# Optimization experiments

Hardware: AMD Instinct MI355X
Metric: run time of the kernel (lower is better)

Reference implementation:

```python
import jax, jax.numpy as jnp
import numpy as np

N_NODES = 100000
N_EDGES = 3200000
IN_DIM = 768
HIDDEN = 128
CLASS_NUM = 2
N_GRAPHS = 512


def setup_inputs() -> dict:
    key = jax.random.key(0)
    ks = jax.random.split(key, 10)
    x = jax.random.normal(ks[0], (N_NODES, IN_DIM), dtype=jnp.float32)
    edge_index = jax.random.randint(ks[1], (2, N_EDGES), 0, N_NODES, dtype=jnp.int64)
    ptr = jnp.sort(jax.random.randint(ks[2], (N_GRAPHS + 1,), 0, N_NODES, dtype=jnp.int64))
    def glorot(k, shape):
        lim = jnp.sqrt(6.0 / (shape[0] + shape[1]))
        return jax.random.uniform(k, shape, jnp.float32, -lim, lim)
    W1 = glorot(ks[3], (IN_DIM, HIDDEN))
    b1 = jnp.zeros((HIDDEN,), jnp.float32)
    W2 = glorot(ks[4], (HIDDEN, HIDDEN))
    b2 = jnp.zeros((HIDDEN,), jnp.float32)
    Wc = glorot(ks[5], (HIDDEN, CLASS_NUM))
    bc = jnp.zeros((CLASS_NUM,), jnp.float32)
    return {"x": x, "edge_index": edge_index, "ptr": ptr,
            "W1": W1, "b1": b1, "W2": W2, "b2": b2, "Wc": Wc, "bc": bc}


def _gcn_conv(x, W, b, src, dst, norm, n_nodes):
    # PyG GCNConv: linear first, then normalized scatter-add aggregation, then bias
    h = x @ W                                  # [N, out]
    msg = h[src] * norm[:, None]               # gather + scale, [E+N, out]
    out = jax.ops.segment_sum(msg, dst, num_segments=n_nodes)
    return out + b


def reference(x, edge_index, ptr, W1, b1, W2, b2, Wc, bc):
    n = x.shape[0]
    loop = jnp.arange(n, dtype=edge_index.dtype)
    src = jnp.concatenate([edge_index[0], loop])  # add self-loops
    dst = jnp.concatenate([edge_index[1], loop])
    deg = jax.ops.segment_sum(jnp.ones_like(dst, dtype=x.dtype), dst, num_segments=n)
    dinv = jnp.where(deg > 0, jax.lax.rsqrt(deg), 0.0)
    norm = dinv[src] * dinv[dst]               # symmetric normalization
    h = jax.nn.relu(_gcn_conv(x, W1, b1, src, dst, norm, n))
    h = jax.nn.relu(_gcn_conv(h, W2, b2, src, dst, norm, n))
    out = _gcn_conv(h, Wc, bc, src, dst, norm, n)
    return out[ptr[:-1]]                       # first_pool: first node of each graph
```

## Files before the change

kernel.cpp:

```cpp
#include <hip/hip_runtime.h>

typedef short bf16x8 __attribute__((ext_vector_type(8)));
typedef float f32x4 __attribute__((ext_vector_type(4)));
typedef _Float16 f16x4 __attribute__((ext_vector_type(4)));

__device__ __forceinline__ unsigned short f2bf_rn(float x) {
    unsigned int u = __float_as_uint(x);
    unsigned int r = u + 0x7FFF + ((u >> 16) & 1);
    return (unsigned short)(r >> 16);
}
__device__ __forceinline__ float bf2f(unsigned short h) {
    return __uint_as_float(((unsigned int)h) << 16);
}


__global__ __launch_bounds__(256) void bucket_hist(const int* __restrict__ ei,
                                                   int* __restrict__ bcnt, int E, int NB) {
    __shared__ int h[1024];
    for (int i = threadIdx.x; i < NB; i += 256) h[i] = 0;
    __syncthreads();
    for (int e = blockIdx.x * blockDim.x + threadIdx.x; e < E; e += gridDim.x * blockDim.x) {
        atomicAdd(&h[ei[E + e] >> 7], 1);
    }
    __syncthreads();
    for (int i = threadIdx.x; i < NB; i += 256) {
        int v = h[i];
        if (v) atomicAdd(&bcnt[i], v);
    }
}

__global__ __launch_bounds__(1024) void bucket_scan(const int* __restrict__ bcnt,
                                                    int* __restrict__ bbase,
                                                    int* __restrict__ bcur,
                                                    int* __restrict__ offs,
                                                    int NB, int NN, int E) {
    __shared__ int s[1024];
    int t = threadIdx.x;
    int v = (t < NB) ? bcnt[t] : 0;
    s[t] = v;
    __syncthreads();
    for (int off = 1; off < 1024; off <<= 1) {
        int u = (t >= off) ? s[t - off] : 0;
        __syncthreads();
        s[t] += u;
        __syncthreads();
    }
    if (t < NB) {
        int base = s[t] - v;
        bbase[t] = base;
        bcur[t] = base;
    }
    if (t == 0) {
        bbase[NB] = E;
        offs[NN] = E;
    }
}

__global__ __launch_bounds__(256) void bucket_scatter(const int* __restrict__ ei,
                                                      int* __restrict__ bcur,
                                                      unsigned int* __restrict__ epk,
                                                      int E, int NB) {
    __shared__ int hist[1024];
    __shared__ int cur[1024];
    int tid = threadIdx.x;
    int chunk = (E + gridDim.x - 1) / gridDim.x;
    int beg = blockIdx.x * chunk;
    int end = beg + chunk; if (end > E) end = E;
    for (int i = tid; i < NB; i += 256) hist[i] = 0;
    __syncthreads();
    for (int e = beg + tid; e < end; e += 256) {
        atomicAdd(&hist[ei[E + e] >> 7], 1);
    }
    __syncthreads();
    for (int i = tid; i < NB; i += 256) {
        int c = hist[i];
        cur[i] = c ? atomicAdd(&bcur[i], c) : 0;
    }
    __syncthreads();
    for (int e = beg + tid; e < end; e += 256) {
        int s = ei[e];
        int d = ei[E + e];
        int p = atomicAdd(&cur[d >> 7], 1);
        epk[p] = ((unsigned)(d & 127) << 17) | (unsigned)s;
    }
}

__global__ __launch_bounds__(256) void bucket_build(const unsigned int* __restrict__ epk,
                                                    const int* __restrict__ bbase,
                                                    int* __restrict__ offs,
                                                    float* __restrict__ dinv,
                                                    int* __restrict__ srt,
                                                    int NN) {
    __shared__ int lcnt[128];
    __shared__ int sc[128];
    __shared__ int lcur[128];
    int b = blockIdx.x;
    int tid = threadIdx.x;
    int base = bbase[b], endp = bbase[b + 1];
    int ne = endp - base;
    int v0 = b << 7;
    int nv = NN - v0; if (nv > 128) nv = 128;

    if (tid < 128) lcnt[tid] = 0;
    __syncthreads();
    for (int i = tid; i < ne; i += 256) {
        int d = (int)(epk[base + i] >> 17);
        atomicAdd(&lcnt[d], 1);
    }
    __syncthreads();
    if (tid < 128) sc[tid] = lcnt[tid];
    __syncthreads();
    for (int off = 1; off < 128; off <<= 1) {
        int u = (tid < 128 && tid >= off) ? sc[tid - off] : 0;
        __syncthreads();
        if (tid < 128) sc[tid] += u;
        __syncthreads();
    }
    if (tid < nv) {
        int ex = sc[tid] - lcnt[tid];
        offs[v0 + tid] = base + ex;
        lcur[tid] = base + ex;
        dinv[v0 + tid] = rsqrtf((float)(lcnt[tid] + 1));
    }
    __syncthreads();
    for (int i = tid; i < ne; i += 256) {
        unsigned int pk = epk[base + i];
        int d = (int)(pk >> 17);
        int s = (int)(pk & 0x1FFFFu);
        int p = atomicAdd(&lcur[d], 1);
        srt[p] = s;
    }
}

__global__ void wt_prep(const float* __restrict__ W, unsigned short* __restrict__ hi,
                        unsigned short* __restrict__ lo, int K) {
    int idx = blockIdx.x * 256 + threadIdx.x;
    if (idx >= K * 128) return;
    int k = idx >> 7;
    int c = idx & 127;
    float x = W[idx];
    unsigned short h = f2bf_rn(x);
    unsigned short l = f2bf_rn(x - bf2f(h));
    hi[(size_t)c * K + k] = h;
    lo[(size_t)c * K + k] = l;
}

template <int K>
__global__ __launch_bounds__(256) void gemm_mfma(const float* __restrict__ X,
                                                 const unsigned short* __restrict__ Wt_hi,
                                                 const unsigned short* __restrict__ Wt_lo,
                                                 const float* __restrict__ dinv,
                                                 _Float16* __restrict__ G, int n) {
    __shared__ unsigned short As_hi[128][40];
    __shared__ unsigned short As_lo[128][40];
    __shared__ unsigned short Bs_hi[128][40];
    __shared__ unsigned short Bs_lo[128][40];

    const int tid = threadIdx.x;
    const int wave = tid >> 6;
    const int lane = tid & 63;
    const int l15 = lane & 15;
    const int l4 = lane >> 4;
    const int row0 = blockIdx.x * 128;
    const int wr0 = wave * 32;

    f32x4 acc[2][8];
#pragma unroll
    for (int i = 0; i < 2; ++i)
#pragma unroll
        for (int j = 0; j < 8; ++j) acc[i][j] = (f32x4){0.f, 0.f, 0.f, 0.f};

    const int sr = tid >> 1;
    const int sf = (tid & 1) * 16;

    for (int k0 = 0; k0 < K; k0 += 32) {
        __syncthreads();
        {
            int grow = row0 + sr;
            float4 v[4];
            if (grow < n) {
                const float* src = X + (size_t)grow * K + k0 + sf;
#pragma unroll
                for (int g = 0; g < 4; ++g) v[g] = *(const float4*)(src + g * 4);
            } else {
#pragma unroll
                for (int g = 0; g < 4; ++g) v[g] = make_float4(0.f, 0.f, 0.f, 0.f);
            }
#pragma unroll
            for (int g = 0; g < 4; ++g) {
                ushort4 h, l;
                h.x = f2bf_rn(v[g].x); l.x = f2bf_rn(v[g].x - bf2f(h.x));
                h.y = f2bf_rn(v[g].y); l.y = f2bf_rn(v[g].y - bf2f(h.y));
                h.z = f2bf_rn(v[g].z); l.z = f2bf_rn(v[g].z - bf2f(h.z));
                h.w = f2bf_rn(v[g].w); l.w = f2bf_rn(v[g].w - bf2f(h.w));
                *(ushort4*)&As_hi[sr][sf + g * 4] = h;
                *(ushort4*)&As_lo[sr][sf + g * 4] = l;
            }
        }
        {
#pragma unroll
            for (int rep = 0; rep < 2; ++rep) {
                int id = tid + rep * 256;
                int c = id >> 2;
                int q = (id & 3) * 8;
                *(uint4*)&Bs_hi[c][q] = *(const uint4*)&Wt_hi[(size_t)c * K + k0 + q];
                *(uint4*)&Bs_lo[c][q] = *(const uint4*)&Wt_lo[(size_t)c * K + k0 + q];
            }
        }
        __syncthreads();
        bf16x8 ah[2], al[2];
#pragma unroll
        for (int i = 0; i < 2; ++i) {
            ah[i] = *(const bf16x8*)&As_hi[wr0 + i * 16 + l15][l4 * 8];
            al[i] = *(const bf16x8*)&As_lo[wr0 + i * 16 + l15][l4 * 8];
        }
#pragma unroll
        for (int j = 0; j < 8; ++j) {
            bf16x8 bh = *(const bf16x8*)&Bs_hi[j * 16 + l15][l4 * 8];
            bf16x8 bl = *(const bf16x8*)&Bs_lo[j * 16 + l15][l4 * 8];
#pragma unroll
            for (int i = 0; i < 2; ++i) {
                acc[i][j] = __builtin_amdgcn_mfma_f32_16x16x32_bf16(ah[i], bh, acc[i][j], 0, 0, 0);
                acc[i][j] = __builtin_amdgcn_mfma_f32_16x16x32_bf16(ah[i], bl, acc[i][j], 0, 0, 0);
                acc[i][j] = __builtin_amdgcn_mfma_f32_16x16x32_bf16(al[i], bh, acc[i][j], 0, 0, 0);
            }
        }
    }
#pragma unroll
    for (int i = 0; i < 2; ++i) {
#pragma unroll
        for (int r = 0; r < 4; ++r) {
            int grow = row0 + wr0 + i * 16 + l4 * 4 + r;
            if (grow < n) {
                float dv = dinv[grow];
#pragma unroll
                for (int j = 0; j < 8; ++j) {
                    G[(size_t)grow * 128 + j * 16 + l15] = (_Float16)(acc[i][j][r] * dv);
                }
            }
        }
    }
}

__global__ __launch_bounds__(256) void aggregate_kernel(const _Float16* __restrict__ G,
                                                        const int* __restrict__ offs,
                                                        const int* __restrict__ srt,
                                                        const float* __restrict__ dinv,
                                                        const float* __restrict__ bias,
                                                        float* __restrict__ H, int n, int do_relu) {
    int wid = (blockIdx.x * blockDim.x + threadIdx.x) >> 6;
    int lane = threadIdx.x & 63;
    if (wid >= n) return;
    int hh = lane >> 5;
    int c4 = (lane & 31) * 4;
    int beg = offs[wid], end = offs[wid + 1];
    float ax = 0.f, ay = 0.f, az = 0.f, aw = 0.f;
    if (!hh) {
        f16x4 s = *(const f16x4*)&G[(size_t)wid * 128 + c4];
        ax = (float)s[0]; ay = (float)s[1]; az = (float)s[2]; aw = (float)s[3];
    }
    int e = beg + hh;
    for (; e + 6 < end; e += 8) {
        int s0 = srt[e], s1 = srt[e + 2], s2 = srt[e + 4], s3 = srt[e + 6];
        f16x4 v0 = *(const f16x4*)&G[(size_t)s0 * 128 + c4];
        f16x4 v1 = *(const f16x4*)&G[(size_t)s1 * 128 + c4];
        f16x4 v2 = *(const f16x4*)&G[(size_t)s2 * 128 + c4];
        f16x4 v3 = *(const f16x4*)&G[(size_t)s3 * 128 + c4];
        ax += (float)v0[0] + (float)v1[0] + (float)v2[0] + (float)v3[0];
        ay += (float)v0[1] + (float)v1[1] + (float)v2[1] + (float)v3[1];
        az += (float)v0[2] + (float)v1[2] + (float)v2[2] + (float)v3[2];
        aw += (float)v0[3] + (float)v1[3] + (float)v2[3] + (float)v3[3];
    }
    for (; e < end; e += 2) {
        int s = srt[e];
        f16x4 v = *(const f16x4*)&G[(size_t)s * 128 + c4];
        ax += (float)v[0]; ay += (float)v[1]; az += (float)v[2]; aw += (float)v[3];
    }
    ax += __shfl_xor(ax, 32);
    ay += __shfl_xor(ay, 32);
    az += __shfl_xor(az, 32);
    aw += __shfl_xor(aw, 32);
    if (!hh) {
        float dv = dinv[wid];
        float4 b = *(const float4*)&bias[c4];
        float4 r;
        r.x = ax * dv + b.x;
        r.y = ay * dv + b.y;
        r.z = az * dv + b.z;
        r.w = aw * dv + b.w;
        if (do_relu) {
            r.x = fmaxf(r.x, 0.f); r.y = fmaxf(r.y, 0.f);
            r.z = fmaxf(r.z, 0.f); r.w = fmaxf(r.w, 0.f);
        }
        *(float4*)&H[(size_t)wid * 128 + c4] = r;
    }
}

__global__ __launch_bounds__(256) void gemm_c2_kernel(const float* __restrict__ H,
                                                      const float* __restrict__ Wc,
                                                      const float* __restrict__ dinv,
                                                      float* __restrict__ G3, int n) {
    int wid = (blockIdx.x * blockDim.x + threadIdx.x) >> 6;
    int lane = threadIdx.x & 63;
    if (wid >= n) return;
    float2 h = *(const float2*)&H[(size_t)wid * 128 + lane * 2];
    float w00 = Wc[lane * 4 + 0];
    float w01 = Wc[lane * 4 + 1];
    float w10 = Wc[lane * 4 + 2];
    float w11 = Wc[lane * 4 + 3];
    float p0 = h.x * w00 + h.y * w10;
    float p1 = h.x * w01 + h.y * w11;
    for (int off = 32; off > 0; off >>= 1) {
        p0 += __shfl_xor(p0, off);
        p1 += __shfl_xor(p1, off);
    }
    if (lane == 0) {
        float dv = dinv[wid];
        G3[(size_t)wid * 2 + 0] = p0 * dv;
        G3[(size_t)wid * 2 + 1] = p1 * dv;
    }
}

__global__ __launch_bounds__(64) void final_kernel(const float* __restrict__ G3,
                                                   const int* __restrict__ ptr,
                                                   const int* __restrict__ offs,
                                                   const int* __restrict__ srt,
                                                   const float* __restrict__ dinv,
                                                   const float* __restrict__ bc,
                                                   float* __restrict__ out, int ngraphs) {
    int i = blockIdx.x;
    if (i >= ngraphs) return;
    int v = ptr[i];
    int lane = threadIdx.x;
    float p0 = 0.f, p1 = 0.f;
    int beg = offs[v], end = offs[v + 1];
    for (int e = beg + lane; e < end; e += 64) {
        int s = srt[e];
        p0 += G3[(size_t)s * 2 + 0];
        p1 += G3[(size_t)s * 2 + 1];
    }
    for (int off = 32; off > 0; off >>= 1) {
        p0 += __shfl_xor(p0, off);
        p1 += __shfl_xor(p1, off);
    }
    if (lane == 0) {
        p0 += G3[(size_t)v * 2 + 0];
        p1 += G3[(size_t)v * 2 + 1];
        float dv = dinv[v];
        out[i * 2 + 0] = p0 * dv + bc[0];
        out[i * 2 + 1] = p1 * dv + bc[1];
    }
}

extern "C" void kernel_launch(void* const* d_in, const int* in_sizes, int n_in,
                              void* d_out, int out_size, void* d_ws, size_t ws_size,
                              hipStream_t stream) {
    const float* x  = (const float*)d_in[0];
    const int* ei   = (const int*)d_in[1];
    const int* ptr  = (const int*)d_in[2];
    const float* W1 = (const float*)d_in[3];
    const float* b1 = (const float*)d_in[4];
    const float* W2 = (const float*)d_in[5];
    const float* b2 = (const float*)d_in[6];
    const float* Wc = (const float*)d_in[7];
    const float* bc = (const float*)d_in[8];
    float* out = (float*)d_out;

    const int IN_DIM = 768, HID = 128;
    const int NN = in_sizes[0] / IN_DIM;
    const int E  = in_sizes[1] / 2;
    const int NG = in_sizes[2] - 1;
    const int NB = (NN + 127) >> 7;

    char* ws = (char*)d_ws;
    size_t off = 0;
    auto alloc = [&](size_t bytes) -> void* {
        void* p = ws + off;
        off += (bytes + 255) & ~(size_t)255;
        return p;
    };
    float* dinv   = (float*)alloc((size_t)NN * 4);
    int*   offs   = (int*)alloc((size_t)(NN + 1) * 4);
    int*   bcnt   = (int*)alloc((size_t)(NB + 1) * 4);
    int*   bbase  = (int*)alloc((size_t)(NB + 1) * 4);
    int*   bcur   = (int*)alloc((size_t)NB * 4);
    int*   srt    = (int*)alloc((size_t)E * 4);
    _Float16* G   = (_Float16*)alloc((size_t)NN * HID * 2);
    float* H      = (float*)alloc((size_t)NN * HID * 4);
    float* G3     = (float*)alloc((size_t)NN * 2 * 4);
    unsigned short* Wt1_hi = (unsigned short*)alloc((size_t)IN_DIM * HID * 2);
    unsigned short* Wt1_lo = (unsigned short*)alloc((size_t)IN_DIM * HID * 2);
    unsigned short* Wt2_hi = (unsigned short*)alloc((size_t)HID * HID * 2);
    unsigned short* Wt2_lo = (unsigned short*)alloc((size_t)HID * HID * 2);

    unsigned int* epk = (unsigned int*)H;

    (void)n_in; (void)out_size; (void)ws_size;

    hipMemsetAsync(bcnt, 0, (size_t)(NB + 1) * 4, stream);
    bucket_hist<<<512, 256, 0, stream>>>(ei, bcnt, E, NB);
    bucket_scan<<<1, 1024, 0, stream>>>(bcnt, bbase, bcur, offs, NB, NN, E);
    bucket_scatter<<<256, 256, 0, stream>>>(ei, bcur, epk, E, NB);
    bucket_build<<<NB, 256, 0, stream>>>(epk, bbase, offs, dinv, srt, NN);

    wt_prep<<<(IN_DIM * HID + 255) / 256, 256, 0, stream>>>(W1, Wt1_hi, Wt1_lo, IN_DIM);
    wt_prep<<<(HID * HID + 255) / 256, 256, 0, stream>>>(W2, Wt2_hi, Wt2_lo, HID);

    int gblocks = (NN + 127) / 128;
    int agg_blocks = (NN * 64 + 255) / 256;

    gemm_mfma<768><<<gblocks, 256, 0, stream>>>(x, Wt1_hi, Wt1_lo, dinv, G, NN);
    aggregate_kernel<<<agg_blocks, 256, 0, stream>>>(G, offs, srt, dinv, b1, H, NN, 1);
    gemm_mfma<128><<<gblocks, 256, 0, stream>>>(H, Wt2_hi, Wt2_lo, dinv, G, NN);
    aggregate_kernel<<<agg_blocks, 256, 0, stream>>>(G, offs, srt, dinv, b2, H, NN, 1);
    gemm_c2_kernel<<<agg_blocks, 256, 0, stream>>>(H, Wc, dinv, G3, NN);
    final_kernel<<<NG, 64, 0, stream>>>(G3, ptr, offs, srt, dinv, bc, out, NG);
}
```

Measured before the change: 520.1 us.

## Store GEMM output in column-sliced planes and aggregate per slice

The GEMM epilogue now writes G as 8 planes of 16 half-precision columns each, instead of row-major 128-wide rows. Aggregation launches 8 blocks per group of 4 nodes, one per column slice, so that concurrently running blocks gather from a smaller 3.2MB plane. The aim is better L2 locality for the random neighbour gathers. In exchange, each gather becomes a 32-byte segment per edge, the CSR index list is read 8 times, and the GEMM epilogue stores are more scattered.

```diff
diff --git a/kernel.cpp b/kernel.cpp
--- a/kernel.cpp
+++ b/kernel.cpp
@@ -2,7 +2,7 @@
 
 typedef short bf16x8 __attribute__((ext_vector_type(8)));
 typedef float f32x4 __attribute__((ext_vector_type(4)));
-typedef _Float16 f16x4 __attribute__((ext_vector_type(4)));
+typedef _Float16 f16x2 __attribute__((ext_vector_type(2)));
 
 __device__ __forceinline__ unsigned short f2bf_rn(float x) {
     unsigned int u = __float_as_uint(x);
@@ -163,6 +163,7 @@
     const int l4 = lane >> 4;
     const int row0 = blockIdx.x * 128;
     const int wr0 = wave * 32;
+    const size_t plane = (size_t)n * 16;
 
     f32x4 acc[2][8];
 #pragma unroll
@@ -235,64 +236,56 @@
                 float dv = dinv[grow];
 #pragma unroll
                 for (int j = 0; j < 8; ++j) {
-                    G[(size_t)grow * 128 + j * 16 + l15] = (_Float16)(acc[i][j][r] * dv);
+                    G[plane * j + (size_t)grow * 16 + l15] = (_Float16)(acc[i][j][r] * dv);
                 }
             }
         }
     }
 }
 
-__global__ __launch_bounds__(256) void aggregate_kernel(const _Float16* __restrict__ G,
-                                                        const int* __restrict__ offs,
-                                                        const int* __restrict__ srt,
-                                                        const float* __restrict__ dinv,
-                                                        const float* __restrict__ bias,
-                                                        float* __restrict__ H, int n, int do_relu) {
-    int wid = (blockIdx.x * blockDim.x + threadIdx.x) >> 6;
+__global__ __launch_bounds__(256) void aggregate_slice(const _Float16* __restrict__ G,
+                                                       const int* __restrict__ offs,
+                                                       const int* __restrict__ srt,
+                                                       const float* __restrict__ dinv,
+                                                       const float* __restrict__ bias,
+                                                       float* __restrict__ H, int n, int do_relu) {
+    int bid = blockIdx.x;
+    int slice = bid & 7;
+    int node = (bid >> 3) * 4 + (threadIdx.x >> 6);
+    if (node >= n) return;
     int lane = threadIdx.x & 63;
-    if (wid >= n) return;
-    int hh = lane >> 5;
-    int c4 = (lane & 31) * 4;
-    int beg = offs[wid], end = offs[wid + 1];
-    float ax = 0.f, ay = 0.f, az = 0.f, aw = 0.f;
-    if (!hh) {
-        f16x4 s = *(const f16x4*)&G[(size_t)wid * 128 + c4];
-        ax = (float)s[0]; ay = (float)s[1]; az = (float)s[2]; aw = (float)s[3];
-    }
-    int e = beg + hh;
-    for (; e + 6 < end; e += 8) {
-        int s0 = srt[e], s1 = srt[e + 2], s2 = srt[e + 4], s3 = srt[e + 6];
-        f16x4 v0 = *(const f16x4*)&G[(size_t)s0 * 128 + c4];
-        f16x4 v1 = *(const f16x4*)&G[(size_t)s1 * 128 + c4];
-        f16x4 v2 = *(const f16x4*)&G[(size_t)s2 * 128 + c4];
-        f16x4 v3 = *(const f16x4*)&G[(size_t)s3 * 128 + c4];
-        ax += (float)v0[0] + (float)v1[0] + (float)v2[0] + (float)v3[0];
-        ay += (float)v0[1] + (float)v1[1] + (float)v2[1] + (float)v3[1];
-        az += (float)v0[2] + (float)v1[2] + (float)v2[2] + (float)v3[2];
-        aw += (float)v0[3] + (float)v1[3] + (float)v2[3] + (float)v3[3];
-    }
-    for (; e < end; e += 2) {
+    int pairId = lane & 7;
+    int slot = lane >> 3;
+    const f16x2* Gp = (const f16x2*)(G + (size_t)slice * (size_t)n * 16);
+    int beg = offs[node], end = offs[node + 1];
+    float a0 = 0.f, a1 = 0.f;
+    int e = beg + slot;
+    for (; e + 8 < end; e += 16) {
+        int s0 = srt[e], s1 = srt[e + 8];
+        f16x2 v0 = Gp[(size_t)s0 * 8 + pairId];
+        f16x2 v1 = Gp[(size_t)s1 * 8 + pairId];
+        a0 += (float)v0[0] + (float)v1[0];
+        a1 += (float)v0[1] + (float)v1[1];
+    }
+    if (e < end) {
         int s = srt[e];
-        f16x4 v = *(const f16x4*)&G[(size_t)s * 128 + c4];
-        ax += (float)v[0]; ay += (float)v[1]; az += (float)v[2]; aw += (float)v[3];
-    }
-    ax += __shfl_xor(ax, 32);
-    ay += __shfl_xor(ay, 32);
-    az += __shfl_xor(az, 32);
-    aw += __shfl_xor(aw, 32);
-    if (!hh) {
-        float dv = dinv[wid];
-        float4 b = *(const float4*)&bias[c4];
-        float4 r;
-        r.x = ax * dv + b.x;
-        r.y = ay * dv + b.y;
-        r.z = az * dv + b.z;
-        r.w = aw * dv + b.w;
-        if (do_relu) {
-            r.x = fmaxf(r.x, 0.f); r.y = fmaxf(r.y, 0.f);
-            r.z = fmaxf(r.z, 0.f); r.w = fmaxf(r.w, 0.f);
-        }
-        *(float4*)&H[(size_t)wid * 128 + c4] = r;
+        f16x2 v = Gp[(size_t)s * 8 + pairId];
+        a0 += (float)v[0];
+        a1 += (float)v[1];
+    }
+    a0 += __shfl_xor(a0, 8);  a1 += __shfl_xor(a1, 8);
+    a0 += __shfl_xor(a0, 16); a1 += __shfl_xor(a1, 16);
+    a0 += __shfl_xor(a0, 32); a1 += __shfl_xor(a1, 32);
+    if (lane < 8) {
+        f16x2 sv = Gp[(size_t)node * 8 + lane];
+        a0 += (float)sv[0];
+        a1 += (float)sv[1];
+        float dv = dinv[node];
+        float2 b = *(const float2*)&bias[slice * 16 + lane * 2];
+        float r0 = a0 * dv + b.x;
+        float r1 = a1 * dv + b.y;
+        if (do_relu) { r0 = fmaxf(r0, 0.f); r1 = fmaxf(r1, 0.f); }
+        *(float2*)&H[(size_t)node * 128 + slice * 16 + lane * 2] = make_float2(r0, r1);
     }
 }
 
@@ -407,12 +400,13 @@
     wt_prep<<<(HID * HID + 255) / 256, 256, 0, stream>>>(W2, Wt2_hi, Wt2_lo, HID);
 
     int gblocks = (NN + 127) / 128;
-    int agg_blocks = (NN * 64 + 255) / 256;
+    int slice_blocks = ((NN + 3) / 4) * 8;
+    int wpn_blocks = (NN * 64 + 255) / 256;
 
     gemm_mfma<768><<<gblocks, 256, 0, stream>>>(x, Wt1_hi, Wt1_lo, dinv, G, NN);
-    aggregate_kernel<<<agg_blocks, 256, 0, stream>>>(G, offs, srt, dinv, b1, H, NN, 1);
+    aggregate_slice<<<slice_blocks, 256, 0, stream>>>(G, offs, srt, dinv, b1, H, NN, 1);
     gemm_mfma<128><<<gblocks, 256, 0, stream>>>(H, Wt2_hi, Wt2_lo, dinv, G, NN);
-    aggregate_kernel<<<agg_blocks, 256, 0, stream>>>(G, offs, srt, dinv, b2, H, NN, 1);
-    gemm_c2_kernel<<<agg_blocks, 256, 0, stream>>>(H, Wc, dinv, G3, NN);
+    aggregate_slice<<<slice_blocks, 256, 0, stream>>>(G, offs, srt, dinv, b2, H, NN, 1);
+    gemm_c2_kernel<<<wpn_blocks, 256, 0, stream>>>(H, Wc, dinv, G3, NN);
     final_kernel<<<NG, 64, 0, stream>>>(G3, ptr, offs, srt, dinv, bc, out, NG);
 }
```

Measured after the change: 829.5 us. 1.59x slower.
